# Kernel optimization log

Hardware: AMD Instinct MI355X
Metric: run time of the kernel (lower is better)

The kernel has to match this reference:

```python
import jax, jax.numpy as jnp
import numpy as np

B, S, D = 1, 4096, 1024
H = 16
HD = D // H  # 64


def setup_inputs() -> dict:
    key = jax.random.key(0)
    k1, k2, k3 = jax.random.split(key, 3)
    x = jax.random.normal(k1, (B, S, D), dtype=jnp.float32)
    W_qkv = jax.random.normal(k2, (D, 3 * D), dtype=jnp.float32) * (1.0 / np.sqrt(D))
    b_qkv = jnp.zeros((3 * D,), dtype=jnp.float32)
    W_out = jax.random.normal(k3, (D, D), dtype=jnp.float32) * (1.0 / np.sqrt(D))
    b_out = jnp.zeros((D,), dtype=jnp.float32)
    return {"x": x, "W_qkv": W_qkv, "b_qkv": b_qkv, "W_out": W_out, "b_out": b_out}


def reference(x, W_qkv, b_qkv, W_out, b_out):
    b, s, d = x.shape
    qkv = x @ W_qkv + b_qkv                      # [b, s, 3d]
    q, k, v = jnp.split(qkv, 3, axis=-1)
    q = q.reshape(b, s, H, HD)
    k = k.reshape(b, s, H, HD)
    v = v.reshape(b, s, H, HD)
    scale = 1.0 / np.sqrt(HD).astype(np.float32)
    scores = jnp.einsum("bqhd,bkhd->bhqk", q, k) * scale  # [b, h, s, s]
    causal = jnp.tril(jnp.ones((s, s), dtype=bool))
    scores = jnp.where(causal, scores, jnp.float32(-jnp.inf))
    attn = jax.nn.softmax(scores, axis=-1)
    out = jnp.einsum("bhqk,bkhd->bqhd", attn, v).reshape(b, s, d)
    return out @ W_out + b_out
```

## Files before the change

kernel.cpp:

```cpp
#include <hip/hip_runtime.h>
#include <cstdint>
#include <cstddef>


typedef __attribute__((ext_vector_type(4))) float f32x4;
typedef __attribute__((ext_vector_type(16))) float f32x16;
typedef __attribute__((ext_vector_type(8))) short s16x8;
typedef __attribute__((ext_vector_type(4))) unsigned u32x4;

#define SM_SCALE_LOG2 0.18033688011112042f

#if __has_builtin(__builtin_amdgcn_exp2f)
#define EXP2(x) __builtin_amdgcn_exp2f(x)
#else
#define EXP2(x) exp2f(x)
#endif

static __device__ __forceinline__ short f2bf(float f) {
  unsigned u = __builtin_bit_cast(unsigned, f);
  u = (u + 0x7fffu + ((u >> 16) & 1u)) >> 16;
  return (short)u;
}

static __device__ __forceinline__ unsigned cvtpk(float lo, float hi) {
  unsigned r;
  asm("v_cvt_pk_bf16_f32 %0, %1, %2" : "=v"(r) : "v"(lo), "v"(hi));
  return r;
}

static __device__ __forceinline__ void plswap(unsigned& a, unsigned& b) {
#if __has_builtin(__builtin_amdgcn_permlane32_swap)
  auto r = __builtin_amdgcn_permlane32_swap((int)a, (int)b, false, false);
  unsigned tmp[2];
  __builtin_memcpy(tmp, &r, 8);
  a = tmp[0];
  b = tmp[1];
#else
  const unsigned xa = (unsigned)__shfl_xor((int)a, 32);
  const unsigned xb = (unsigned)__shfl_xor((int)b, 32);
  const bool hiL = (threadIdx.x & 32) != 0;
  const unsigned na = hiL ? xb : a;
  const unsigned nb = hiL ? b : xa;
  a = na;
  b = nb;
#endif
}

static __device__ __forceinline__ void gload16(const void* g, void* l) {
  __builtin_amdgcn_global_load_lds((const __attribute__((address_space(1))) void*)g,
                                   (__attribute__((address_space(3))) void*)l, 16, 0, 0);
}

#define MFMA32(A, B, C) __builtin_amdgcn_mfma_f32_32x32x16_bf16(A, B, C, 0, 0, 0)

__global__ __launch_bounds__(256) void convx_k(const float* __restrict__ x,
                                               short* __restrict__ xb) {
  const size_t i = ((size_t)blockIdx.x * 256 + threadIdx.x) * 8;
  float4 a = *(const float4*)(x + i);
  float4 b = *(const float4*)(x + i + 4);
  u32x4 p;
  p[0] = cvtpk(a.x, a.y); p[1] = cvtpk(a.z, a.w);
  p[2] = cvtpk(b.x, b.y); p[3] = cvtpk(b.z, b.w);
  *(u32x4*)(xb + i) = p;
}

__global__ __launch_bounds__(256, 2) void convT_k(const float* __restrict__ W,
                                                  short* __restrict__ Wt, int K, int N) {
  __shared__ short T[64][72];
  const int t = threadIdx.x;
  const int n0 = blockIdx.x * 64, k0 = blockIdx.y * 64;
  const int kr = t >> 2, c0 = (t & 3) * 16;
  const float* src = W + (size_t)(k0 + kr) * N + n0 + c0;
  float4 v0 = *(const float4*)(src + 0);
  float4 v1 = *(const float4*)(src + 4);
  float4 v2 = *(const float4*)(src + 8);
  float4 v3 = *(const float4*)(src + 12);
  T[c0 + 0][kr] = f2bf(v0.x);  T[c0 + 1][kr] = f2bf(v0.y);
  T[c0 + 2][kr] = f2bf(v0.z);  T[c0 + 3][kr] = f2bf(v0.w);
  T[c0 + 4][kr] = f2bf(v1.x);  T[c0 + 5][kr] = f2bf(v1.y);
  T[c0 + 6][kr] = f2bf(v1.z);  T[c0 + 7][kr] = f2bf(v1.w);
  T[c0 + 8][kr] = f2bf(v2.x);  T[c0 + 9][kr] = f2bf(v2.y);
  T[c0 + 10][kr] = f2bf(v2.z); T[c0 + 11][kr] = f2bf(v2.w);
  T[c0 + 12][kr] = f2bf(v3.x); T[c0 + 13][kr] = f2bf(v3.y);
  T[c0 + 14][kr] = f2bf(v3.z); T[c0 + 15][kr] = f2bf(v3.w);
  __syncthreads();
  const int nr = t >> 2, kc = (t & 3) * 16;
  s16x8 a = *(const s16x8*)&T[nr][kc];
  s16x8 b = *(const s16x8*)&T[nr][kc + 8];
  short* dst = Wt + (size_t)(n0 + nr) * K + k0 + kc;
  *(s16x8*)dst = a;
  *(s16x8*)(dst + 8) = b;
}

template <int ABF, int SCAT>
__global__ __launch_bounds__(256, 2) void gemm_k(
    const void* __restrict__ Ap, const short* __restrict__ Bt,
    const float* __restrict__ bias,
    short* __restrict__ q_ws, short* __restrict__ k_ws, short* __restrict__ vt_ws,
    float* __restrict__ out, int N, int K) {
  constexpr int LDA = ABF ? 32 : 40;
  __shared__ short As[2][128 * LDA];
  __shared__ short Bs[2][128 * 32];

  const int t = threadIdx.x, l = t & 63, w = t >> 6;
  const int wm = (w >> 1) * 64, wn = (w & 1) * 64;
  const int m0 = blockIdx.x * 128, n0 = blockIdx.y * 128;
  const int lr = l & 15, lh = l >> 4;

  f32x4 acc[4][4];
#pragma unroll
  for (int i = 0; i < 4; i++)
#pragma unroll
    for (int j = 0; j < 4; j++) acc[i][j] = (f32x4){0.f, 0.f, 0.f, 0.f};

  const int arow = t >> 1, ac0 = (t & 1) * 16;
  const int grow = l >> 2, gc0 = (l & 3) * 8;

  auto stage = [&](int b, int kt) {
    {
      const int r0 = w * 32;
      const short* s0 = Bt + (size_t)(n0 + r0 + grow) * K + kt + gc0;
      gload16(s0, &Bs[b][r0 * 32]);
      gload16(s0 + (size_t)16 * K, &Bs[b][(r0 + 16) * 32]);
    }
    if constexpr (ABF) {
      const int r0 = w * 32;
      const short* s0 = (const short*)Ap + (size_t)(m0 + r0 + grow) * K + kt + gc0;
      gload16(s0, &As[b][r0 * 32]);
      gload16(s0 + (size_t)16 * K, &As[b][(r0 + 16) * 32]);
    } else {
      const float* ap = (const float*)Ap + (size_t)(m0 + arow) * K + kt + ac0;
      float4 v0 = *(const float4*)(ap + 0);
      float4 v1 = *(const float4*)(ap + 4);
      float4 v2 = *(const float4*)(ap + 8);
      float4 v3 = *(const float4*)(ap + 12);
      u32x4 p0, p1;
      p0[0] = cvtpk(v0.x, v0.y); p0[1] = cvtpk(v0.z, v0.w);
      p0[2] = cvtpk(v1.x, v1.y); p0[3] = cvtpk(v1.z, v1.w);
      p1[0] = cvtpk(v2.x, v2.y); p1[1] = cvtpk(v2.z, v2.w);
      p1[2] = cvtpk(v3.x, v3.y); p1[3] = cvtpk(v3.z, v3.w);
      *(u32x4*)&As[b][arow * LDA + ac0] = p0;
      *(u32x4*)&As[b][arow * LDA + ac0 + 8] = p1;
    }
  };

  const int nt = K >> 5;
  stage(0, 0);
  __syncthreads();
  int cur = 0;
  for (int tt = 0; tt < nt; tt++) {
    if (tt + 1 < nt) stage(cur ^ 1, (tt + 1) * 32);
    s16x8 af[4], bfv[4];
#pragma unroll
    for (int mi = 0; mi < 4; mi++)
      af[mi] = *(const s16x8*)&As[cur][(wm + mi * 16 + lr) * LDA + lh * 8];
#pragma unroll
    for (int ni = 0; ni < 4; ni++)
      bfv[ni] = *(const s16x8*)&Bs[cur][(wn + ni * 16 + lr) * 32 + lh * 8];
#pragma unroll
    for (int mi = 0; mi < 4; mi++)
#pragma unroll
      for (int ni = 0; ni < 4; ni++)
        acc[mi][ni] = __builtin_amdgcn_mfma_f32_16x16x32_bf16(af[mi], bfv[ni],
                                                              acc[mi][ni], 0, 0, 0);
    __syncthreads();
    cur ^= 1;
  }

#pragma unroll
  for (int mi = 0; mi < 4; mi++) {
#pragma unroll
    for (int ni = 0; ni < 4; ni++) {
      const int gn = n0 + wn + ni * 16 + lr;
      const float bb = bias[gn];
      if constexpr (SCAT) {
        const int sect = gn >> 10, dd = gn & 1023, hh = dd >> 6, hd = dd & 63;
#pragma unroll
        for (int j = 0; j < 4; j++) {
          const int gm = m0 + wm + mi * 16 + lh * 4 + j;
          const short bv = f2bf(acc[mi][ni][j] + bb);
          if (sect == 0)
            q_ws[((size_t)hh * 4096 + gm) * 64 + hd] = bv;
          else if (sect == 1)
            k_ws[(((size_t)hh * 128 + (gm >> 5)) * 32 + (gm & 31)) * 64 + hd] = bv;
          else
            vt_ws[(((size_t)hh * 128 + (gm >> 5)) * 64 + hd) * 32 + (gm & 31)] = bv;
        }
      } else {
#pragma unroll
        for (int j = 0; j < 4; j++) {
          const int gm = m0 + wm + mi * 16 + lh * 4 + j;
          out[(size_t)gm * N + gn] = acc[mi][ni][j] + bb;
        }
      }
    }
  }
}

__global__ __launch_bounds__(256, 3) void attn_k(
    const short* __restrict__ q_ws, const short* __restrict__ k_ws,
    const short* __restrict__ vt2, short* __restrict__ o_ws) {
  __shared__ float accO[32][64];
  __shared__ float mls[4][2][32];
  __shared__ float lsS[32];

  const int tid = threadIdx.x, l = tid & 63, w = tid >> 6;
  const int ql = l & 31, hi = l >> 5;
  const int h = blockIdx.y;
  const int p = blockIdx.x;

  f32x16 po0, po1;
  float m, ls;
  s16x8 qf0, qf1, qf2, qf3;
  s16x8 kf0, kf1, kf2, kf3;

  auto phase = [&](int s, int t0, int t1) {
#pragma unroll
    for (int r = 0; r < 16; r++) { po0[r] = 0.f; po1[r] = 0.f; }
    m = -1e30f;
    ls = 0.f;
    {
      const short* qp = q_ws + ((size_t)h * 4096 + 32 * s + ql) * 64 + hi * 8;
      qf0 = *(const s16x8*)(qp);
      qf1 = *(const s16x8*)(qp + 16);
      qf2 = *(const s16x8*)(qp + 32);
      qf3 = *(const s16x8*)(qp + 48);
    }
    if (t0 < t1) {
      const short* kb = k_ws + (size_t)h * 262144 + (size_t)t0 * 2048 + ql * 64 + hi * 8;
      const short* vb = vt2 + (size_t)h * 262144 + (size_t)t0 * 2048 + ql * 32 + hi * 8;
      kf0 = *(const s16x8*)(kb);
      kf1 = *(const s16x8*)(kb + 16);
      kf2 = *(const s16x8*)(kb + 32);
      kf3 = *(const s16x8*)(kb + 48);
      kb += 2048;
      for (int tt = t0; tt < t1; tt++) {
        s16x8 vf0 = *(const s16x8*)(vb);
        s16x8 vf1 = *(const s16x8*)(vb + 16);
        s16x8 vf2 = *(const s16x8*)(vb + 1024);
        s16x8 vf3 = *(const s16x8*)(vb + 1040);
        vb += 2048;
        f32x16 sa;
#pragma unroll
        for (int r = 0; r < 16; r++) sa[r] = 0.f;
        sa = MFMA32(kf0, qf0, sa);
        sa = MFMA32(kf1, qf1, sa);
        sa = MFMA32(kf2, qf2, sa);
        sa = MFMA32(kf3, qf3, sa);
        kf0 = *(const s16x8*)(kb);
        kf1 = *(const s16x8*)(kb + 16);
        kf2 = *(const s16x8*)(kb + 32);
        kf3 = *(const s16x8*)(kb + 48);
        kb += 2048;
        if (tt == s) {
#pragma unroll
          for (int r = 0; r < 16; r++) {
            const int kvl = (r & 3) + 8 * (r >> 2) + 4 * hi;
            if (kvl > ql) sa[r] = -3e38f;
          }
        }
        const float x0 = fmaxf(fmaxf(sa[0], sa[1]), fmaxf(sa[2], sa[3]));
        const float x1 = fmaxf(fmaxf(sa[4], sa[5]), fmaxf(sa[6], sa[7]));
        const float x2 = fmaxf(fmaxf(sa[8], sa[9]), fmaxf(sa[10], sa[11]));
        const float x3 = fmaxf(fmaxf(sa[12], sa[13]), fmaxf(sa[14], sa[15]));
        float pm = fmaxf(fmaxf(x0, x1), fmaxf(x2, x3));
        pm = fmaxf(pm, __shfl_xor(pm, 32));
        pm *= SM_SCALE_LOG2;
        if (!__all(pm <= m + 8.0f)) {
          const float nm = fmaxf(m, pm);
          const float corr = EXP2(m - nm);
          m = nm;
          ls *= corr;
#pragma unroll
          for (int r = 0; r < 16; r++) {
            const int qr = (r & 3) + 8 * (r >> 2) + 4 * hi;
            const float cq = __shfl(corr, qr);
            po0[r] *= cq;
            po1[r] *= cq;
          }
        }
        float e[16];
#pragma unroll
        for (int r = 0; r < 16; r++) e[r] = EXP2(__builtin_fmaf(sa[r], SM_SCALE_LOG2, -m));
        float rs = ((e[0] + e[1]) + (e[2] + e[3])) + ((e[4] + e[5]) + (e[6] + e[7])) +
                   (((e[8] + e[9]) + (e[10] + e[11])) + ((e[12] + e[13]) + (e[14] + e[15])));
        rs += __shfl_xor(rs, 32);
        ls += rs;
        unsigned pk0 = cvtpk(e[0], e[1]), pk1 = cvtpk(e[2], e[3]);
        unsigned pk2 = cvtpk(e[4], e[5]), pk3 = cvtpk(e[6], e[7]);
        unsigned pk4 = cvtpk(e[8], e[9]), pk5 = cvtpk(e[10], e[11]);
        unsigned pk6 = cvtpk(e[12], e[13]), pk7 = cvtpk(e[14], e[15]);
        plswap(pk0, pk2);
        plswap(pk1, pk3);
        plswap(pk4, pk6);
        plswap(pk5, pk7);
        const u32x4 pw0 = {pk0, pk1, pk2, pk3};
        const u32x4 pw1 = {pk4, pk5, pk6, pk7};
        const s16x8 pa0 = __builtin_bit_cast(s16x8, pw0);
        const s16x8 pa1 = __builtin_bit_cast(s16x8, pw1);
        po0 = MFMA32(pa0, vf0, po0);
        po0 = MFMA32(pa1, vf1, po0);
        po1 = MFMA32(pa0, vf2, po1);
        po1 = MFMA32(pa1, vf3, po1);
      }
    }
    if (hi == 0) {
      mls[w][0][ql] = m;
      mls[w][1][ql] = ls;
    }
    __syncthreads();
    {
      const float ms = fmaxf(fmaxf(mls[0][0][ql], mls[1][0][ql]),
                             fmaxf(mls[2][0][ql], mls[3][0][ql]));
      const float lss = mls[0][1][ql] * EXP2(mls[0][0][ql] - ms) +
                        mls[1][1][ql] * EXP2(mls[1][0][ql] - ms) +
                        mls[2][1][ql] * EXP2(mls[2][0][ql] - ms) +
                        mls[3][1][ql] * EXP2(mls[3][0][ql] - ms);
      if (w == 0 && hi == 0) lsS[ql] = lss;
    }
#pragma unroll
    for (int r = 0; r < 16; r++) {
      const int qr = (r & 3) + 8 * (r >> 2) + 4 * hi;
      const float msq = fmaxf(fmaxf(mls[0][0][qr], mls[1][0][qr]),
                              fmaxf(mls[2][0][qr], mls[3][0][qr]));
      const float er = EXP2(mls[w][0][qr] - msq);
      po0[r] *= er;
      po1[r] *= er;
    }
#pragma unroll
    for (int wv = 0; wv < 4; wv++) {
      if (w == wv) {
#pragma unroll
        for (int r = 0; r < 16; r++) {
          const int qr = (r & 3) + 8 * (r >> 2) + 4 * hi;
          if (wv == 0) {
            accO[qr][ql] = po0[r];
            accO[qr][32 + ql] = po1[r];
          } else {
            accO[qr][ql] += po0[r];
            accO[qr][32 + ql] += po1[r];
          }
        }
      }
      __syncthreads();
    }
    {
      const int qo = tid >> 3, d0 = (tid & 7) * 8;
      const float inv = 1.0f / lsS[qo];
      s16x8 ov;
#pragma unroll
      for (int j = 0; j < 8; j++) ov[j] = f2bf(accO[qo][d0 + j] * inv);
      *(s16x8*)(o_ws + (size_t)(32 * s + qo) * 1024 + h * 64 + d0) = ov;
    }
    __syncthreads();
  };

  const int ntA = p + 1, ntB = 128 - p;
  phase(p, (ntA * w) >> 2, (ntA * (w + 1)) >> 2);
  phase(127 - p, (ntB * (3 - w)) >> 2, (ntB * (4 - w)) >> 2);
}

extern "C" void kernel_launch(void* const* d_in, const int* in_sizes, int n_in,
                              void* d_out, int out_size, void* d_ws, size_t ws_size,
                              hipStream_t stream) {
  const float* x     = (const float*)d_in[0];
  const float* W_qkv = (const float*)d_in[1];
  const float* b_qkv = (const float*)d_in[2];
  const float* W_out = (const float*)d_in[3];
  const float* b_out = (const float*)d_in[4];
  float* out = (float*)d_out;

  short* R0    = (short*)d_ws;
  short* q_ws  = R0 + (size_t)4 * 1024 * 1024;
  short* k_ws  = q_ws + (size_t)4 * 1024 * 1024;
  short* vt_ws = k_ws + (size_t)4 * 1024 * 1024;
  short* Wo_t  = vt_ws;
  short* xbf   = vt_ws + (size_t)4 * 1024 * 1024;

  const bool big_ws = ws_size >= (size_t)40 * 1024 * 1024;

  convT_k<<<dim3(48, 16), 256, 0, stream>>>(W_qkv, R0, 1024, 3072);
  if (big_ws) {
    convx_k<<<2048, 256, 0, stream>>>(x, xbf);
    gemm_k<1, 1><<<dim3(32, 24), 256, 0, stream>>>(xbf, R0, b_qkv, q_ws, k_ws,
                                                   vt_ws, nullptr, 3072, 1024);
  } else {
    gemm_k<0, 1><<<dim3(32, 24), 256, 0, stream>>>(x, R0, b_qkv, q_ws, k_ws,
                                                   vt_ws, nullptr, 3072, 1024);
  }
  attn_k<<<dim3(64, 16), 256, 0, stream>>>(q_ws, k_ws, vt_ws, R0);
  convT_k<<<dim3(16, 16), 256, 0, stream>>>(W_out, Wo_t, 1024, 1024);
  gemm_k<1, 0><<<dim3(32, 8), 256, 0, stream>>>(R0, Wo_t, b_out, nullptr, nullptr,
                                                nullptr, out, 1024, 1024);
}
```

Measured before the change: 251.1 us.

## Stage K/V tiles through double-buffered LDS with swizzled layouts in attention

The attention kernel now processes 64-query blocks with four waves (two query halves by two KV halves) and cooperatively loads 64-row K and V^T tiles into double-buffered shared memory via async global-to-LDS loads, instead of each wave streaming its own K/V fragments from global memory. The QKV GEMM epilogue writes K and V^T in new XOR-swizzled row-major layouts to avoid LDS bank conflicts. The grid is remapped to 512 blocks pairing causal blocks for load balance, with a simpler two-way softmax merge. This trades more LDS use and per-tile barriers for reuse of K/V across query rows.

```diff
diff --git a/kernel.cpp b/kernel.cpp
--- a/kernel.cpp
+++ b/kernel.cpp
@@ -182,9 +182,9 @@
           if (sect == 0)
             q_ws[((size_t)hh * 4096 + gm) * 64 + hd] = bv;
           else if (sect == 1)
-            k_ws[(((size_t)hh * 128 + (gm >> 5)) * 32 + (gm & 31)) * 64 + hd] = bv;
+            k_ws[((size_t)hh * 4096 + gm) * 64 + (hd ^ ((gm & 7) << 3))] = bv;
           else
-            vt_ws[(((size_t)hh * 128 + (gm >> 5)) * 64 + hd) * 32 + (gm & 31)] = bv;
+            vt_ws[((size_t)hh * 64 + hd) * 4096 + (gm ^ ((hd & 7) << 3))] = bv;
         }
       } else {
 #pragma unroll
@@ -199,64 +199,70 @@
 
 __global__ __launch_bounds__(256, 3) void attn_k(
     const short* __restrict__ q_ws, const short* __restrict__ k_ws,
-    const short* __restrict__ vt2, short* __restrict__ o_ws) {
-  __shared__ float accO[32][64];
-  __shared__ float mls[4][2][32];
-  __shared__ float lsS[32];
+    const short* __restrict__ vt_ws, short* __restrict__ o_ws) {
+  __shared__ short Ks[2][64 * 64];
+  __shared__ short Vts[2][64 * 64];
+  __shared__ float accO[64][64];
+  __shared__ float mls[2][2][64];
 
   const int tid = threadIdx.x, l = tid & 63, w = tid >> 6;
+  const int sid = w & 1, kh = w >> 1;
   const int ql = l & 31, hi = l >> 5;
-  const int h = blockIdx.y;
-  const int p = blockIdx.x;
-
-  f32x16 po0, po1;
-  float m, ls;
-  s16x8 qf0, qf1, qf2, qf3;
-  s16x8 kf0, kf1, kf2, kf3;
-
-  auto phase = [&](int s, int t0, int t1) {
+  const int lin = blockIdx.x;
+  const int logical = (lin & 7) * 64 + (lin >> 3);
+  const int pair = logical & 31;
+  const int h = logical >> 5;
+  const int gl8 = l >> 3, gc8 = (l & 7) * 8;
+
+  auto run = [&](int qb) {
+    const int q0w = qb + 32 * sid;
+    const int qg = q0w + ql;
+    const int nt = (qb >> 6) + 1;
+
+    s16x8 qf[4];
+    {
+      const short* qp = q_ws + ((size_t)h * 4096 + qg) * 64 + hi * 8;
+      qf[0] = *(const s16x8*)qp;
+      qf[1] = *(const s16x8*)(qp + 16);
+      qf[2] = *(const s16x8*)(qp + 32);
+      qf[3] = *(const s16x8*)(qp + 48);
+    }
+
+    f32x16 po0, po1;
 #pragma unroll
     for (int r = 0; r < 16; r++) { po0[r] = 0.f; po1[r] = 0.f; }
-    m = -1e30f;
-    ls = 0.f;
-    {
-      const short* qp = q_ws + ((size_t)h * 4096 + 32 * s + ql) * 64 + hi * 8;
-      qf0 = *(const s16x8*)(qp);
-      qf1 = *(const s16x8*)(qp + 16);
-      qf2 = *(const s16x8*)(qp + 32);
-      qf3 = *(const s16x8*)(qp + 48);
-    }
-    if (t0 < t1) {
-      const short* kb = k_ws + (size_t)h * 262144 + (size_t)t0 * 2048 + ql * 64 + hi * 8;
-      const short* vb = vt2 + (size_t)h * 262144 + (size_t)t0 * 2048 + ql * 32 + hi * 8;
-      kf0 = *(const s16x8*)(kb);
-      kf1 = *(const s16x8*)(kb + 16);
-      kf2 = *(const s16x8*)(kb + 32);
-      kf3 = *(const s16x8*)(kb + 48);
-      kb += 2048;
-      for (int tt = t0; tt < t1; tt++) {
-        s16x8 vf0 = *(const s16x8*)(vb);
-        s16x8 vf1 = *(const s16x8*)(vb + 16);
-        s16x8 vf2 = *(const s16x8*)(vb + 1024);
-        s16x8 vf3 = *(const s16x8*)(vb + 1040);
-        vb += 2048;
+    float m = -1e30f, ls = 0.f;
+
+    auto stage = [&](int b, int tt) {
+      const short* kb = k_ws + ((size_t)h * 4096 + (size_t)tt * 64 + w * 16 + gl8) * 64 + gc8;
+      gload16(kb, &Ks[b][w * 16 * 64]);
+      gload16(kb + (size_t)8 * 64, &Ks[b][(w * 16 + 8) * 64]);
+      const short* vb = vt_ws + ((size_t)h * 64 + w * 16 + gl8) * 4096 + (size_t)tt * 64 + gc8;
+      gload16(vb, &Vts[b][w * 16 * 64]);
+      gload16(vb + (size_t)8 * 4096, &Vts[b][(w * 16 + 8) * 64]);
+    };
+
+    stage(0, 0);
+    __syncthreads();
+    int cur = 0;
+    for (int tt = 0; tt < nt; tt++) {
+      if (tt + 1 < nt) stage(cur ^ 1, tt + 1);
+      const int kv0w = tt * 64 + kh * 32;
+      if (kv0w <= q0w + 31) {
+        const int row = kh * 32 + ql;
         f32x16 sa;
 #pragma unroll
         for (int r = 0; r < 16; r++) sa[r] = 0.f;
-        sa = MFMA32(kf0, qf0, sa);
-        sa = MFMA32(kf1, qf1, sa);
-        sa = MFMA32(kf2, qf2, sa);
-        sa = MFMA32(kf3, qf3, sa);
-        kf0 = *(const s16x8*)(kb);
-        kf1 = *(const s16x8*)(kb + 16);
-        kf2 = *(const s16x8*)(kb + 32);
-        kf3 = *(const s16x8*)(kb + 48);
-        kb += 2048;
-        if (tt == s) {
+#pragma unroll
+        for (int ks2 = 0; ks2 < 4; ks2++) {
+          s16x8 kf = *(const s16x8*)&Ks[cur][row * 64 + ((ks2 * 16 + hi * 8) ^ ((ql & 7) << 3))];
+          sa = MFMA32(kf, qf[ks2], sa);
+        }
+        if (kv0w + 31 > q0w) {
 #pragma unroll
           for (int r = 0; r < 16; r++) {
             const int kvl = (r & 3) + 8 * (r >> 2) + 4 * hi;
-            if (kvl > ql) sa[r] = -3e38f;
+            if (kv0w + kvl > qg) sa[r] = -3e38f;
           }
         }
         const float x0 = fmaxf(fmaxf(sa[0], sa[1]), fmaxf(sa[2], sa[3]));
@@ -298,66 +304,80 @@
         const u32x4 pw1 = {pk4, pk5, pk6, pk7};
         const s16x8 pa0 = __builtin_bit_cast(s16x8, pw0);
         const s16x8 pa1 = __builtin_bit_cast(s16x8, pw1);
-        po0 = MFMA32(pa0, vf0, po0);
-        po0 = MFMA32(pa1, vf1, po0);
-        po1 = MFMA32(pa0, vf2, po1);
-        po1 = MFMA32(pa1, vf3, po1);
-      }
-    }
-    if (hi == 0) {
-      mls[w][0][ql] = m;
-      mls[w][1][ql] = ls;
-    }
-    __syncthreads();
-    {
-      const float ms = fmaxf(fmaxf(mls[0][0][ql], mls[1][0][ql]),
-                             fmaxf(mls[2][0][ql], mls[3][0][ql]));
-      const float lss = mls[0][1][ql] * EXP2(mls[0][0][ql] - ms) +
-                        mls[1][1][ql] * EXP2(mls[1][0][ql] - ms) +
-                        mls[2][1][ql] * EXP2(mls[2][0][ql] - ms) +
-                        mls[3][1][ql] * EXP2(mls[3][0][ql] - ms);
-      if (w == 0 && hi == 0) lsS[ql] = lss;
-    }
-#pragma unroll
-    for (int r = 0; r < 16; r++) {
-      const int qr = (r & 3) + 8 * (r >> 2) + 4 * hi;
-      const float msq = fmaxf(fmaxf(mls[0][0][qr], mls[1][0][qr]),
-                              fmaxf(mls[2][0][qr], mls[3][0][qr]));
-      const float er = EXP2(mls[w][0][qr] - msq);
-      po0[r] *= er;
-      po1[r] *= er;
-    }
-#pragma unroll
-    for (int wv = 0; wv < 4; wv++) {
-      if (w == wv) {
-#pragma unroll
-        for (int r = 0; r < 16; r++) {
-          const int qr = (r & 3) + 8 * (r >> 2) + 4 * hi;
-          if (wv == 0) {
-            accO[qr][ql] = po0[r];
-            accO[qr][32 + ql] = po1[r];
-          } else {
-            accO[qr][ql] += po0[r];
-            accO[qr][32 + ql] += po1[r];
-          }
-        }
+        const int kidx0 = (kh * 32 + hi * 8) ^ ((ql & 7) << 3);
+        const int kidx1 = (kh * 32 + 16 + hi * 8) ^ ((ql & 7) << 3);
+        s16x8 vf00 = *(const s16x8*)&Vts[cur][ql * 64 + kidx0];
+        s16x8 vf01 = *(const s16x8*)&Vts[cur][ql * 64 + kidx1];
+        s16x8 vf10 = *(const s16x8*)&Vts[cur][(32 + ql) * 64 + kidx0];
+        s16x8 vf11 = *(const s16x8*)&Vts[cur][(32 + ql) * 64 + kidx1];
+        po0 = MFMA32(pa0, vf00, po0);
+        po0 = MFMA32(pa1, vf01, po0);
+        po1 = MFMA32(pa0, vf10, po1);
+        po1 = MFMA32(pa1, vf11, po1);
       }
       __syncthreads();
-    }
+      cur ^= 1;
+    }
+
+    const int qloc = sid * 32 + ql;
+    if (hi == 0) {
+      mls[kh][0][qloc] = m;
+      mls[kh][1][qloc] = ls;
+    }
+    __syncthreads();
+    float er[16];
+#pragma unroll
+    for (int r = 0; r < 16; r++) {
+      const int qr = sid * 32 + (r & 3) + 8 * (r >> 2) + 4 * hi;
+      const float mt = fmaxf(mls[0][0][qr], mls[1][0][qr]);
+      er[r] = EXP2(mls[kh][0][qr] - mt);
+    }
+    if (kh == 0) {
+#pragma unroll
+      for (int r = 0; r < 16; r++) {
+        const int qr = sid * 32 + (r & 3) + 8 * (r >> 2) + 4 * hi;
+        accO[qr][ql] = po0[r] * er[r];
+        accO[qr][32 + ql] = po1[r] * er[r];
+      }
+    }
+    __syncthreads();
+    if (kh == 1) {
+#pragma unroll
+      for (int r = 0; r < 16; r++) {
+        const int qr = sid * 32 + (r & 3) + 8 * (r >> 2) + 4 * hi;
+        accO[qr][ql] += po0[r] * er[r];
+        accO[qr][32 + ql] += po1[r] * er[r];
+      }
+    }
+    __syncthreads();
     {
-      const int qo = tid >> 3, d0 = (tid & 7) * 8;
-      const float inv = 1.0f / lsS[qo];
-      s16x8 ov;
-#pragma unroll
-      for (int j = 0; j < 8; j++) ov[j] = f2bf(accO[qo][d0 + j] * inv);
-      *(s16x8*)(o_ws + (size_t)(32 * s + qo) * 1024 + h * 64 + d0) = ov;
+      const int qo = tid >> 2, d0 = (tid & 3) * 16;
+      const float m0v = mls[0][0][qo], m1v = mls[1][0][qo];
+      const float mt = fmaxf(m0v, m1v);
+      const float lst = mls[0][1][qo] * EXP2(m0v - mt) + mls[1][1][qo] * EXP2(m1v - mt);
+      const float inv = 1.0f / lst;
+      const f32x4 a0 = *(const f32x4*)&accO[qo][d0];
+      const f32x4 a1 = *(const f32x4*)&accO[qo][d0 + 4];
+      const f32x4 a2 = *(const f32x4*)&accO[qo][d0 + 8];
+      const f32x4 a3 = *(const f32x4*)&accO[qo][d0 + 12];
+      s16x8 ov0, ov1;
+      ov0[0] = f2bf(a0[0] * inv); ov0[1] = f2bf(a0[1] * inv);
+      ov0[2] = f2bf(a0[2] * inv); ov0[3] = f2bf(a0[3] * inv);
+      ov0[4] = f2bf(a1[0] * inv); ov0[5] = f2bf(a1[1] * inv);
+      ov0[6] = f2bf(a1[2] * inv); ov0[7] = f2bf(a1[3] * inv);
+      ov1[0] = f2bf(a2[0] * inv); ov1[1] = f2bf(a2[1] * inv);
+      ov1[2] = f2bf(a2[2] * inv); ov1[3] = f2bf(a2[3] * inv);
+      ov1[4] = f2bf(a3[0] * inv); ov1[5] = f2bf(a3[1] * inv);
+      ov1[6] = f2bf(a3[2] * inv); ov1[7] = f2bf(a3[3] * inv);
+      short* op = o_ws + (size_t)(qb + qo) * 1024 + h * 64 + d0;
+      *(s16x8*)op = ov0;
+      *(s16x8*)(op + 8) = ov1;
     }
     __syncthreads();
   };
 
-  const int ntA = p + 1, ntB = 128 - p;
-  phase(p, (ntA * w) >> 2, (ntA * (w + 1)) >> 2);
-  phase(127 - p, (ntB * (3 - w)) >> 2, (ntB * (4 - w)) >> 2);
+  run(pair * 64);
+  run((63 - pair) * 64);
 }
 
 extern "C" void kernel_launch(void* const* d_in, const int* in_sizes, int n_in,
@@ -388,7 +408,7 @@
     gemm_k<0, 1><<<dim3(32, 24), 256, 0, stream>>>(x, R0, b_qkv, q_ws, k_ws,
                                                    vt_ws, nullptr, 3072, 1024);
   }
-  attn_k<<<dim3(64, 16), 256, 0, stream>>>(q_ws, k_ws, vt_ws, R0);
+  attn_k<<<512, 256, 0, stream>>>(q_ws, k_ws, vt_ws, R0);
   convT_k<<<dim3(16, 16), 256, 0, stream>>>(W_out, Wo_t, 1024, 1024);
   gemm_k<1, 0><<<dim3(32, 8), 256, 0, stream>>>(R0, Wo_t, b_out, nullptr, nullptr,
                                                 nullptr, out, 1024, 1024);
```

Measured after the change: 218.8 us. 12.8% less time.
